# Performance work log

Measured on AMD Instinct MI355X. Metric: run time of the kernel, lower is better.

## Reference

```python
import jax, jax.numpy as jnp
import numpy as np

N = 50000      # n_nodes
E = 800000     # n_edges
D = 128        # input feature dim
H = 8          # num_heads
U = 32         # units per head
SLOPE = 0.2    # keras leaky_relu default negative_slope
EPS = 1e-7


def setup_inputs() -> dict:
    key = jax.random.key(0)
    k0, k1, k2, k3 = jax.random.split(key, 4)
    x = jax.random.normal(k0, (N, D), dtype=jnp.float32)
    edges = jax.random.randint(k1, (E, 2), 0, N, dtype=jnp.int32)
    kernel = jax.random.normal(k2, (D, H * U), dtype=jnp.float32) * 0.05
    kernel_attention1 = jax.random.normal(k3, (1, H, U), dtype=jnp.float32) * 0.05
    bias_attention = jnp.zeros((1, H, U), dtype=jnp.float32)
    bias = jnp.zeros((H * U,), dtype=jnp.float32)
    return {
        "x": x,
        "edges": edges,
        "kernel": kernel,
        "kernel_attention1": kernel_attention1,
        "bias_attention": bias_attention,
        "bias": bias,
    }


def reference(x, edges, kernel, kernel_attention1, bias_attention, bias):
    targets = edges[:, 1]
    sources = edges[:, 0]
    # node transform: [N, D] @ [D, H*U] -> [N, H, U]
    xp = (x @ kernel).reshape(-1, H, U)
    xbias = xp + bias_attention  # use_v2 + use_bias path
    # GATv2 attention: gather endpoints, leaky_relu, project with attention kernel
    f = xbias[targets] + xbias[sources]            # [E, H, U]
    scores = jnp.sum(jax.nn.leaky_relu(f, SLOPE) * kernel_attention1, axis=-1)  # [E, H]
    # segment softmax over incoming edges of each target node
    smax = jax.ops.segment_max(scores, targets, num_segments=N)   # [N, H]
    scores = jnp.exp(scores - smax[targets])
    ssum = jax.ops.segment_sum(scores, targets, num_segments=N) + EPS
    scores = scores / ssum[targets]
    # weighted scatter-sum aggregation
    out = jax.ops.segment_sum(scores[..., None] * xp[sources], targets, num_segments=N)  # [N, H, U]
    out = out.reshape(-1, H * U) + bias
    return jax.nn.elu(out)
```

## Files before the change

### kernel.cpp

```cpp
#include <hip/hip_runtime.h>
#include <math.h>

#define NN 50000
#define NE 800000
#define DD 128
#define HU 256
#define SLOPE 0.2f
#define EPSV 1e-7f
#define SCAN_B 1024
#define NBLK ((NN + SCAN_B - 1) / SCAN_B)

typedef __attribute__((ext_vector_type(8))) short short8;
typedef __attribute__((ext_vector_type(4))) float f32x4;

__device__ __forceinline__ float bf2f(unsigned short u) {
  union { unsigned int i; float f; } v; v.i = ((unsigned int)u) << 16; return v.f;
}
__device__ __forceinline__ unsigned short f2bf(float f) {
  union { float ff; unsigned int i; } v; v.ff = f;
  unsigned int r = v.i + 0x7FFFu + ((v.i >> 16) & 1u);
  return (unsigned short)(r >> 16);
}

__global__ __launch_bounds__(256) void prep_kernel(
    const float* __restrict__ kern, unsigned short* __restrict__ kernbT)
{
  int i = blockIdx.x * 256 + threadIdx.x;
  int col = i & 255, k = i >> 8;
  kernbT[(size_t)col * DD + k] = f2bf(kern[(size_t)k * HU + col]);
}

__global__ __launch_bounds__(256) void gemm_mfma_kernel(
    const float* __restrict__ x, const unsigned short* __restrict__ kernbT,
    unsigned short* __restrict__ xpb)
{
  __shared__ __align__(16) unsigned char ldsA[64 * 256];
  __shared__ __align__(16) unsigned char ldsB[128 * 256];
  const int tid = threadIdx.x;
  const int r0 = blockIdx.x * 64;

#pragma unroll
  for (int c = 0; c < 4; ++c) {
    int cc = tid + 256 * c;
    int row = cc >> 4;
    int kp  = (cc & 15) * 8;
    float4 va = make_float4(0.f,0.f,0.f,0.f), vb = va;
    if (r0 + row < NN) {
      const float* g = x + (size_t)(r0 + row) * DD + kp;
      va = *(const float4*)g; vb = *(const float4*)(g + 4);
    }
    uint4 u;
    u.x = (unsigned)f2bf(va.x) | ((unsigned)f2bf(va.y) << 16);
    u.y = (unsigned)f2bf(va.z) | ((unsigned)f2bf(va.w) << 16);
    u.z = (unsigned)f2bf(vb.x) | ((unsigned)f2bf(vb.y) << 16);
    u.w = (unsigned)f2bf(vb.z) | ((unsigned)f2bf(vb.w) << 16);
    *(uint4*)(ldsA + row * 256 + ((kp * 2) ^ ((row & 7) << 4))) = u;
  }
  __syncthreads();

  const int lane = tid & 63, wv = tid >> 6;
  const int arow = wv * 16 + (lane & 15);
  const int kb = (lane >> 4) * 16;
  short8 af[4];
#pragma unroll
  for (int ks = 0; ks < 4; ++ks) {
    int kbyte = ks * 64 + kb;
    af[ks] = *(const short8*)(ldsA + arow * 256 + (kbyte ^ ((arow & 7) << 4)));
  }

  f32x4 acc[16];
#pragma unroll
  for (int i = 0; i < 16; ++i) acc[i] = (f32x4){0.f, 0.f, 0.f, 0.f};

#pragma unroll
  for (int hb = 0; hb < 2; ++hb) {
    __syncthreads();
#pragma unroll
    for (int c = 0; c < 8; ++c) {
      int cc = tid + 256 * c;
      int col = cc >> 4;
      int kp  = (cc & 15) * 8;
      uint4 u = *(const uint4*)(kernbT + (size_t)(hb * 128 + col) * DD + kp);
      *(uint4*)(ldsB + col * 256 + ((kp * 2) ^ ((col & 7) << 4))) = u;
    }
    __syncthreads();
#pragma unroll
    for (int ks = 0; ks < 4; ++ks) {
      int kbyte = ks * 64 + kb;
#pragma unroll
      for (int n = 0; n < 8; ++n) {
        int colL = n * 16 + (lane & 15);
        short8 bf = *(const short8*)(ldsB + colL * 256 + (kbyte ^ ((colL & 7) << 4)));
        acc[hb * 8 + n] = __builtin_amdgcn_mfma_f32_16x16x32_bf16(
            af[ks], bf, acc[hb * 8 + n], 0, 0, 0);
      }
    }
  }

#pragma unroll
  for (int n16 = 0; n16 < 16; ++n16) {
    int col = n16 * 16 + (lane & 15);
#pragma unroll
    for (int r = 0; r < 4; ++r) {
      int row = r0 + wv * 16 + (lane >> 4) * 4 + r;
      if (row < NN) xpb[(size_t)row * HU + col] = f2bf(acc[n16][r]);
    }
  }
}

__global__ __launch_bounds__(256) void hist_kernel(
    const int* __restrict__ edges, int* __restrict__ cnt, int* __restrict__ posw)
{
  int e = blockIdx.x * 256 + threadIdx.x;
  if (e < NE) {
    int2 ed = ((const int2*)edges)[e];
    posw[e] = atomicAdd(&cnt[ed.y], 1);
  }
}

__global__ __launch_bounds__(1024) void scan1_kernel(
    const int* __restrict__ cnt, int* __restrict__ excl, int* __restrict__ btot)
{
  __shared__ int ws[16];
  const int tid = threadIdx.x, lane = tid & 63, wid = tid >> 6;
  const int i = blockIdx.x * SCAN_B + tid;
  int v = (i < NN) ? cnt[i] : 0;
  int sum = v;
#pragma unroll
  for (int off = 1; off < 64; off <<= 1) {
    int n = __shfl_up(sum, off, 64);
    if (lane >= off) sum += n;
  }
  if (lane == 63) ws[wid] = sum;
  __syncthreads();
  int wpre = 0;
  for (int w = 0; w < wid; ++w) wpre += ws[w];
  if (i < NN) excl[i] = wpre + sum - v;
  if (tid == SCAN_B - 1) btot[blockIdx.x] = wpre + sum;
}

__global__ __launch_bounds__(1024) void scan3_kernel(
    const int* __restrict__ excl, const int* __restrict__ btot,
    int* __restrict__ rowptr)
{
  __shared__ int s_off;
  const int tid = threadIdx.x;
  if (tid < 64) {
    int v = (tid < NBLK && tid < (int)blockIdx.x) ? btot[tid] : 0;
#pragma unroll
    for (int o = 32; o; o >>= 1) v += __shfl_xor(v, o, 64);
    if (tid == 0) s_off = v;
    if (blockIdx.x == NBLK - 1) {
      int g = (tid < NBLK) ? btot[tid] : 0;
#pragma unroll
      for (int o = 32; o; o >>= 1) g += __shfl_xor(g, o, 64);
      if (tid == 0) rowptr[NN] = g;
    }
  }
  __syncthreads();
  const int i = blockIdx.x * SCAN_B + tid;
  if (i < NN) rowptr[i] = excl[i] + s_off;
}

__global__ __launch_bounds__(256) void scatter_kernel(
    const int* __restrict__ edges, const int* __restrict__ rowptr,
    const int* __restrict__ posw, int* __restrict__ srcidx)
{
  int e = blockIdx.x * 256 + threadIdx.x;
  if (e < NE) {
    int2 ed = ((const int2*)edges)[e];
    srcidx[rowptr[ed.y] + posw[e]] = ed.x;
  }
}

__global__ __launch_bounds__(256) void aggregate_kernel(
    const unsigned short* __restrict__ xpb, const int* __restrict__ rowptr,
    const int* __restrict__ srcidx, const float* __restrict__ b_att,
    const float* __restrict__ k_att, const float* __restrict__ bias,
    float* __restrict__ out)
{
  const int t = blockIdx.x * 4 + (threadIdx.x >> 6);
  if (t >= NN) return;
  const int l = threadIdx.x & 63;
  const int hu = l * 4;

  const ushort4 xtu = *(const ushort4*)(xpb + (size_t)t * HU + hu);
  const float4 ba = *(const float4*)(b_att + hu);
  const float4 ka = *(const float4*)(k_att + hu);
  const float xtbx = bf2f(xtu.x) + 2.f * ba.x;
  const float xtby = bf2f(xtu.y) + 2.f * ba.y;
  const float xtbz = bf2f(xtu.z) + 2.f * ba.z;
  const float xtbw = bf2f(xtu.w) + 2.f * ba.w;

  const int beg = rowptr[t];
  const int end = rowptr[t + 1];

  float sigma = 0.f;
  float4 acc = make_float4(0.f, 0.f, 0.f, 0.f);

  ushort4 rA = make_ushort4(0, 0, 0, 0), rB = rA;
  if (beg < end)
    rA = *(const ushort4*)(xpb + (size_t)srcidx[beg] * HU + hu);
  if (beg + 1 < end)
    rB = *(const ushort4*)(xpb + (size_t)srcidx[beg + 1] * HU + hu);

  for (int j = beg; j < end; ++j) {
    const ushort4 cu = rA;
    rA = rB;
    if (j + 2 < end)
      rB = *(const ushort4*)(xpb + (size_t)srcidx[j + 2] * HU + hu);

    const float xsx = bf2f(cu.x), xsy = bf2f(cu.y);
    const float xsz = bf2f(cu.z), xsw = bf2f(cu.w);
    float fx = xtbx + xsx;
    float fy = xtby + xsy;
    float fz = xtbz + xsz;
    float fw = xtbw + xsw;
    fx = fmaxf(fx, SLOPE * fx);
    fy = fmaxf(fy, SLOPE * fy);
    fz = fmaxf(fz, SLOPE * fz);
    fw = fmaxf(fw, SLOPE * fw);
    float p = fmaf(fx, ka.x, fmaf(fy, ka.y, fmaf(fz, ka.z, fw * ka.w)));
    p += __shfl_xor(p, 1, 64);
    p += __shfl_xor(p, 2, 64);
    p += __shfl_xor(p, 4, 64);

    const float w = __expf(p);
    sigma += w;
    acc.x = fmaf(w, xsx, acc.x);
    acc.y = fmaf(w, xsy, acc.y);
    acc.z = fmaf(w, xsz, acc.z);
    acc.w = fmaf(w, xsw, acc.w);
  }

  const float inv = 1.f / (sigma + EPSV);
  const float4 bs = *(const float4*)(bias + hu);
  float ox = fmaf(acc.x, inv, bs.x);
  float oy = fmaf(acc.y, inv, bs.y);
  float oz = fmaf(acc.z, inv, bs.z);
  float ow = fmaf(acc.w, inv, bs.w);
  ox = (ox > 0.f) ? ox : (__expf(ox) - 1.f);
  oy = (oy > 0.f) ? oy : (__expf(oy) - 1.f);
  oz = (oz > 0.f) ? oz : (__expf(oz) - 1.f);
  ow = (ow > 0.f) ? ow : (__expf(ow) - 1.f);
  *(float4*)(out + (size_t)t * HU + hu) = make_float4(ox, oy, oz, ow);
}

extern "C" void kernel_launch(void* const* d_in, const int* in_sizes, int n_in,
                              void* d_out, int out_size, void* d_ws, size_t ws_size,
                              hipStream_t stream)
{
  const float* x     = (const float*)d_in[0];
  const int*   edges = (const int*)d_in[1];
  const float* kern  = (const float*)d_in[2];
  const float* katt  = (const float*)d_in[3];
  const float* batt  = (const float*)d_in[4];
  const float* bias  = (const float*)d_in[5];
  float* out = (float*)d_out;

  char* ws = (char*)d_ws;
  size_t off = 0;
  auto alignup = [](size_t v) { return (v + 255) & ~(size_t)255; };
  unsigned short* xpb = (unsigned short*)(ws + off); off = alignup(off + (size_t)NN * HU * sizeof(unsigned short));
  int* cnt    = (int*)(ws + off); off = alignup(off + (size_t)NN * sizeof(int));
  int* rowptr = (int*)(ws + off); off = alignup(off + ((size_t)NN + 8) * sizeof(int));
  int* srcidx = (int*)(ws + off); off = alignup(off + (size_t)NE * sizeof(int));
  int* excl   = (int*)(ws + off); off = alignup(off + (size_t)NN * sizeof(int));
  int* btot   = (int*)(ws + off); off = alignup(off + 64 * sizeof(int));
  int* posw   = (int*)(ws + off); off = alignup(off + (size_t)NE * sizeof(int));
  unsigned short* kernbT = (unsigned short*)(ws + off); off = alignup(off + (size_t)DD * HU * sizeof(unsigned short));

  hipMemsetAsync(cnt, 0, (size_t)NN * sizeof(int), stream);

  prep_kernel<<<128, 256, 0, stream>>>(kern, kernbT);
  gemm_mfma_kernel<<<(NN + 63) / 64, 256, 0, stream>>>(x, kernbT, xpb);
  hist_kernel<<<(NE + 255) / 256, 256, 0, stream>>>(edges, cnt, posw);
  scan1_kernel<<<NBLK, SCAN_B, 0, stream>>>(cnt, excl, btot);
  scan3_kernel<<<NBLK, SCAN_B, 0, stream>>>(excl, btot, rowptr);
  scatter_kernel<<<(NE + 255) / 256, 256, 0, stream>>>(edges, rowptr, posw, srcidx);
  aggregate_kernel<<<(NN + 3) / 4, 256, 0, stream>>>(xpb, rowptr, srcidx, batt, katt, bias, out);
}
```

Before: 252.0 us.

## Split aggregate wavefront into two half-waves processing alternate edges with DPP reductions

The aggregate kernel now has each half of a 64-lane wave process alternate incoming edges, with each lane handling 8 bf16 features loaded as 16-byte vectors. The per-head dot-product reduction moves from three cross-lane shuffles to two DPP quad adds, and the two half-wave partial sums are combined with a single xor-32 shuffle at the end. The separate memset of the count array is folded into the prep kernel. This targets gather latency and shuffle overhead per edge, at the cost of a final cross-half reduction and idle half-waves on low-degree nodes.

After: 224.4 us. -10.9%, faster.

```diff
diff --git a/kernel.cpp b/kernel.cpp
--- a/kernel.cpp
+++ b/kernel.cpp
@@ -21,13 +21,31 @@
   unsigned int r = v.i + 0x7FFFu + ((v.i >> 16) & 1u);
   return (unsigned short)(r >> 16);
 }
+__device__ __forceinline__ float bflo(unsigned int u) {
+  union { unsigned int i; float f; } v; v.i = u << 16; return v.f;
+}
+__device__ __forceinline__ float bfhi(unsigned int u) {
+  union { unsigned int i; float f; } v; v.i = u & 0xFFFF0000u; return v.f;
+}
+template <int CTRL>
+__device__ __forceinline__ float qadd(float p) {
+  int pi = __builtin_bit_cast(int, p);
+  int q = __builtin_amdgcn_update_dpp(pi, pi, CTRL, 0xF, 0xF, false);
+  return p + __builtin_bit_cast(float, q);
+}
+#define DPP_XOR1 0xB1
+#define DPP_XOR2 0x4E
 
 __global__ __launch_bounds__(256) void prep_kernel(
-    const float* __restrict__ kern, unsigned short* __restrict__ kernbT)
+    const float* __restrict__ kern, unsigned short* __restrict__ kernbT,
+    int* __restrict__ cnt)
 {
   int i = blockIdx.x * 256 + threadIdx.x;
-  int col = i & 255, k = i >> 8;
-  kernbT[(size_t)col * DD + k] = f2bf(kern[(size_t)k * HU + col]);
+  if (i < DD * HU) {
+    int col = i & 255, k = i >> 8;
+    kernbT[(size_t)col * DD + k] = f2bf(kern[(size_t)k * HU + col]);
+  }
+  for (int c = i; c < NN; c += 128 * 256) cnt[c] = 0;
 }
 
 __global__ __launch_bounds__(256) void gemm_mfma_kernel(
@@ -182,68 +200,79 @@
   const int t = blockIdx.x * 4 + (threadIdx.x >> 6);
   if (t >= NN) return;
   const int l = threadIdx.x & 63;
-  const int hu = l * 4;
-
-  const ushort4 xtu = *(const ushort4*)(xpb + (size_t)t * HU + hu);
-  const float4 ba = *(const float4*)(b_att + hu);
-  const float4 ka = *(const float4*)(k_att + hu);
-  const float xtbx = bf2f(xtu.x) + 2.f * ba.x;
-  const float xtby = bf2f(xtu.y) + 2.f * ba.y;
-  const float xtbz = bf2f(xtu.z) + 2.f * ba.z;
-  const float xtbw = bf2f(xtu.w) + 2.f * ba.w;
-
-  const int beg = rowptr[t];
-  const int end = rowptr[t + 1];
-
+  const int half = l >> 5;
+  const int hl = l & 31;
+  const int hu = hl * 8;
+
+  const uint4 xtu = *(const uint4*)(xpb + (size_t)t * HU + hu);
+  const float4 ka0 = *(const float4*)(k_att + hu);
+  const float4 ka1 = *(const float4*)(k_att + hu + 4);
+  const float4 ba0 = *(const float4*)(b_att + hu);
+  const float4 ba1 = *(const float4*)(b_att + hu + 4);
+  float xtb[8], ka[8];
+  xtb[0] = bflo(xtu.x) + 2.f * ba0.x;  xtb[1] = bfhi(xtu.x) + 2.f * ba0.y;
+  xtb[2] = bflo(xtu.y) + 2.f * ba0.z;  xtb[3] = bfhi(xtu.y) + 2.f * ba0.w;
+  xtb[4] = bflo(xtu.z) + 2.f * ba1.x;  xtb[5] = bfhi(xtu.z) + 2.f * ba1.y;
+  xtb[6] = bflo(xtu.w) + 2.f * ba1.z;  xtb[7] = bfhi(xtu.w) + 2.f * ba1.w;
+  ka[0] = ka0.x; ka[1] = ka0.y; ka[2] = ka0.z; ka[3] = ka0.w;
+  ka[4] = ka1.x; ka[5] = ka1.y; ka[6] = ka1.z; ka[7] = ka1.w;
+
+  const int beg = rowptr[t], end = rowptr[t + 1];
   float sigma = 0.f;
-  float4 acc = make_float4(0.f, 0.f, 0.f, 0.f);
-
-  ushort4 rA = make_ushort4(0, 0, 0, 0), rB = rA;
-  if (beg < end)
-    rA = *(const ushort4*)(xpb + (size_t)srcidx[beg] * HU + hu);
-  if (beg + 1 < end)
-    rB = *(const ushort4*)(xpb + (size_t)srcidx[beg + 1] * HU + hu);
-
-  for (int j = beg; j < end; ++j) {
-    const ushort4 cu = rA;
-    rA = rB;
-    if (j + 2 < end)
-      rB = *(const ushort4*)(xpb + (size_t)srcidx[j + 2] * HU + hu);
-
-    const float xsx = bf2f(cu.x), xsy = bf2f(cu.y);
-    const float xsz = bf2f(cu.z), xsw = bf2f(cu.w);
-    float fx = xtbx + xsx;
-    float fy = xtby + xsy;
-    float fz = xtbz + xsz;
-    float fw = xtbw + xsw;
-    fx = fmaxf(fx, SLOPE * fx);
-    fy = fmaxf(fy, SLOPE * fy);
-    fz = fmaxf(fz, SLOPE * fz);
-    fw = fmaxf(fw, SLOPE * fw);
-    float p = fmaf(fx, ka.x, fmaf(fy, ka.y, fmaf(fz, ka.z, fw * ka.w)));
-    p += __shfl_xor(p, 1, 64);
-    p += __shfl_xor(p, 2, 64);
-    p += __shfl_xor(p, 4, 64);
+  float acc[8];
+#pragma unroll
+  for (int c = 0; c < 8; ++c) acc[c] = 0.f;
+
+  int j = beg + half;
+  uint4 r0 = make_uint4(0, 0, 0, 0), r1 = r0;
+  if (j < end)     r0 = *(const uint4*)(xpb + (size_t)srcidx[j]     * HU + hu);
+  if (j + 2 < end) r1 = *(const uint4*)(xpb + (size_t)srcidx[j + 2] * HU + hu);
+
+  for (; j < end; j += 2) {
+    const uint4 cu = r0;
+    r0 = r1;
+    if (j + 4 < end) r1 = *(const uint4*)(xpb + (size_t)srcidx[j + 4] * HU + hu);
+
+    float xs[8];
+    xs[0] = bflo(cu.x); xs[1] = bfhi(cu.x);
+    xs[2] = bflo(cu.y); xs[3] = bfhi(cu.y);
+    xs[4] = bflo(cu.z); xs[5] = bfhi(cu.z);
+    xs[6] = bflo(cu.w); xs[7] = bfhi(cu.w);
+
+    float p = 0.f;
+#pragma unroll
+    for (int c = 0; c < 8; ++c) {
+      float f = xtb[c] + xs[c];
+      f = fmaxf(f, SLOPE * f);
+      p = fmaf(f, ka[c], p);
+    }
+    p = qadd<DPP_XOR1>(p);
+    p = qadd<DPP_XOR2>(p);
 
     const float w = __expf(p);
     sigma += w;
-    acc.x = fmaf(w, xsx, acc.x);
-    acc.y = fmaf(w, xsy, acc.y);
-    acc.z = fmaf(w, xsz, acc.z);
-    acc.w = fmaf(w, xsw, acc.w);
-  }
-
-  const float inv = 1.f / (sigma + EPSV);
-  const float4 bs = *(const float4*)(bias + hu);
-  float ox = fmaf(acc.x, inv, bs.x);
-  float oy = fmaf(acc.y, inv, bs.y);
-  float oz = fmaf(acc.z, inv, bs.z);
-  float ow = fmaf(acc.w, inv, bs.w);
-  ox = (ox > 0.f) ? ox : (__expf(ox) - 1.f);
-  oy = (oy > 0.f) ? oy : (__expf(oy) - 1.f);
-  oz = (oz > 0.f) ? oz : (__expf(oz) - 1.f);
-  ow = (ow > 0.f) ? ow : (__expf(ow) - 1.f);
-  *(float4*)(out + (size_t)t * HU + hu) = make_float4(ox, oy, oz, ow);
+#pragma unroll
+    for (int c = 0; c < 8; ++c) acc[c] = fmaf(w, xs[c], acc[c]);
+  }
+
+#pragma unroll
+  for (int c = 0; c < 8; ++c) acc[c] += __shfl_xor(acc[c], 32, 64);
+  sigma += __shfl_xor(sigma, 32, 64);
+
+  if (half == 0) {
+    const float inv = 1.f / (sigma + EPSV);
+    const float4 bs0 = *(const float4*)(bias + hu);
+    const float4 bs1 = *(const float4*)(bias + hu + 4);
+    const float bsa[8] = {bs0.x, bs0.y, bs0.z, bs0.w, bs1.x, bs1.y, bs1.z, bs1.w};
+    float o[8];
+#pragma unroll
+    for (int c = 0; c < 8; ++c) {
+      float v = fmaf(acc[c], inv, bsa[c]);
+      o[c] = (v > 0.f) ? v : (__expf(v) - 1.f);
+    }
+    *(float4*)(out + (size_t)t * HU + hu)     = make_float4(o[0], o[1], o[2], o[3]);
+    *(float4*)(out + (size_t)t * HU + hu + 4) = make_float4(o[4], o[5], o[6], o[7]);
+  }
 }
 
 extern "C" void kernel_launch(void* const* d_in, const int* in_sizes, int n_in,
@@ -270,9 +299,7 @@
   int* posw   = (int*)(ws + off); off = alignup(off + (size_t)NE * sizeof(int));
   unsigned short* kernbT = (unsigned short*)(ws + off); off = alignup(off + (size_t)DD * HU * sizeof(unsigned short));
 
-  hipMemsetAsync(cnt, 0, (size_t)NN * sizeof(int), stream);
-
-  prep_kernel<<<128, 256, 0, stream>>>(kern, kernbT);
+  prep_kernel<<<128, 256, 0, stream>>>(kern, kernbT, cnt);
   gemm_mfma_kernel<<<(NN + 63) / 64, 256, 0, stream>>>(x, kernbT, xpb);
   hist_kernel<<<(NE + 255) / 256, 256, 0, stream>>>(edges, cnt, posw);
   scan1_kernel<<<NBLK, SCAN_B, 0, stream>>>(cnt, excl, btot);
```
